# Kernel optimization log

Measured on AMD Instinct MI355X. Metric: run time of the kernel, lower is better.

The kernel has to match this reference:

```python
import jax, jax.numpy as jnp
import numpy as np

B, C, H, W = 8, 128, 128, 128
HEADS = 8

def setup_inputs() -> dict:
    key = jax.random.key(0)
    k1, k2 = jax.random.split(key)
    x1 = jax.random.normal(k1, (B, C, H, W), dtype=jnp.float32)
    x2 = jax.random.normal(k2, (B, C, H, W), dtype=jnp.float32)
    return {"x1": x1, "x2": x2}

def reference(x1, x2):
    b, c, h, w = x1.shape
    n = h * w
    hk = c // HEADS  # head key channels
    hv = c // HEADS  # head value channels
    # [B,C,N] layouts (channels-first, as in torch after transpose back)
    vals = x1.reshape(b, c, n)   # values come from x1
    kq = x2.reshape(b, c, n)     # keys and queries come from x2
    k = kq.reshape(b, HEADS, hk, n)
    v = vals.reshape(b, HEADS, hv, n)
    key_sm = jax.nn.softmax(k, axis=-1)   # softmax over N (torch dim=2)
    query_sm = jax.nn.softmax(k, axis=2)  # softmax over head channels (torch dim=1)
    # context = key @ value^T : [B,h,hk,hv]
    context = jnp.einsum('bhkn,bhvn->bhkv', key_sm, v)
    # attended = context^T @ query : [B,h,hv,N]
    attended = jnp.einsum('bhkv,bhkn->bhvn', context, query_sm)
    return attended.reshape(b, c, H, W)
```

## Files before the change

### kernel.cpp

```cpp
#include <hip/hip_runtime.h>
#include <math.h>

#define N_     16384
#define N4     4096
#define BHN    64
#define CH     16
#define CHUNKS 16

#define WS_PART 0
#define WS_ZP   (BHN * CHUNKS * 256)

typedef __attribute__((ext_vector_type(8))) short short8;
typedef __attribute__((ext_vector_type(4))) float f32x4;

static __device__ __forceinline__ short f2bf(float f) {
    __bf16 b = (__bf16)f;
    return __builtin_bit_cast(short, b);
}

__global__ __launch_bounds__(256) void k_ctx_mfma(const float* __restrict__ x1,
                                                  const float* __restrict__ x2,
                                                  float* __restrict__ ws) {
    int chunk = blockIdx.x;
    int bh    = blockIdx.y;
    int tid   = threadIdx.x;
    int w = tid >> 6, l = tid & 63;

    __shared__ __align__(16) short e_s[16][1032];
    __shared__ __align__(16) short v_s[16][1032];
    __shared__ float cred[4][256];
    __shared__ float zs[16];

    const float* xb2 = x2 + (size_t)bh * CH * N_ + chunk * 1024;
    const float* xb1 = x1 + (size_t)bh * CH * N_ + chunk * 1024;

    {
        int row = 4 * w;
        const float4* src = (const float4*)(xb2 + (size_t)row * N_);
        float4 a0 = src[l], a1 = src[64 + l], a2 = src[128 + l], a3 = src[192 + l];
        #pragma unroll
        for (int rr = 0; rr < 4; ++rr) {
            float4 b0 = a0, b1 = a1, b2 = a2, b3 = a3;
            if (rr < 3) {
                const float4* nx = (const float4*)(xb2 + (size_t)(row + rr + 1) * N_);
                a0 = nx[l]; a1 = nx[64 + l]; a2 = nx[128 + l]; a3 = nx[192 + l];
            }
            int r = row + rr;
            float e[16];
            e[0]=__expf(b0.x); e[1]=__expf(b0.y); e[2]=__expf(b0.z); e[3]=__expf(b0.w);
            e[4]=__expf(b1.x); e[5]=__expf(b1.y); e[6]=__expf(b1.z); e[7]=__expf(b1.w);
            e[8]=__expf(b2.x); e[9]=__expf(b2.y); e[10]=__expf(b2.z); e[11]=__expf(b2.w);
            e[12]=__expf(b3.x); e[13]=__expf(b3.y); e[14]=__expf(b3.z); e[15]=__expf(b3.w);
            float z = 0.f;
            #pragma unroll
            for (int i = 0; i < 16; ++i) z += e[i];
            #pragma unroll
            for (int off = 1; off < 64; off <<= 1) z += __shfl_xor(z, off);
            if (l == 0) zs[r] = z;
            #pragma unroll
            for (int s = 0; s < 4; ++s) {
                short4 pk = make_short4(f2bf(e[s*4]), f2bf(e[s*4+1]),
                                        f2bf(e[s*4+2]), f2bf(e[s*4+3]));
                *(short4*)&e_s[r][s * 256 + l * 4] = pk;
            }
        }
    }
    {
        int row = 4 * w;
        const float4* src = (const float4*)(xb1 + (size_t)row * N_);
        float4 a0 = src[l], a1 = src[64 + l], a2 = src[128 + l], a3 = src[192 + l];
        #pragma unroll
        for (int rr = 0; rr < 4; ++rr) {
            float4 b0 = a0, b1 = a1, b2 = a2, b3 = a3;
            if (rr < 3) {
                const float4* nx = (const float4*)(xb1 + (size_t)(row + rr + 1) * N_);
                a0 = nx[l]; a1 = nx[64 + l]; a2 = nx[128 + l]; a3 = nx[192 + l];
            }
            int r = row + rr;
            *(short4*)&v_s[r][0 * 256 + l * 4] = make_short4(f2bf(b0.x), f2bf(b0.y), f2bf(b0.z), f2bf(b0.w));
            *(short4*)&v_s[r][1 * 256 + l * 4] = make_short4(f2bf(b1.x), f2bf(b1.y), f2bf(b1.z), f2bf(b1.w));
            *(short4*)&v_s[r][2 * 256 + l * 4] = make_short4(f2bf(b2.x), f2bf(b2.y), f2bf(b2.z), f2bf(b2.w));
            *(short4*)&v_s[r][3 * 256 + l * 4] = make_short4(f2bf(b3.x), f2bf(b3.y), f2bf(b3.z), f2bf(b3.w));
        }
    }
    __syncthreads();

    int row16 = l & 15;
    int q     = l >> 4;
    f32x4 acc = {0.f, 0.f, 0.f, 0.f};
    #pragma unroll
    for (int s = 0; s < 8; ++s) {
        int col = w * 256 + s * 32 + q * 8;
        short8 af = *(const short8*)&e_s[row16][col];
        short8 bv = *(const short8*)&v_s[row16][col];
        acc = __builtin_amdgcn_mfma_f32_16x16x32_bf16(af, bv, acc, 0, 0, 0);
    }

    #pragma unroll
    for (int r = 0; r < 4; ++r)
        cred[w][(q * 4 + r) * 16 + row16] = acc[r];
    __syncthreads();

    if (tid < 16)
        ws[WS_ZP + (bh * CHUNKS + chunk) * 16 + tid] = zs[tid];
    float c = (cred[0][tid] + cred[1][tid]) + (cred[2][tid] + cred[3][tid]);
    ws[WS_PART + (size_t)(bh * CHUNKS + chunk) * 256 + tid] = c;
}

__global__ __launch_bounds__(256) void k_attend(const float* __restrict__ x2,
                                                const float* __restrict__ ws,
                                                float* __restrict__ out) {
    int cb  = blockIdx.x;
    int bh  = blockIdx.y;
    int tid = threadIdx.x;

    __shared__ float q_s[16][256];
    __shared__ float ctxs[256];
    __shared__ float rzs[16];

    float csum = 0.f;
    #pragma unroll
    for (int c = 0; c < CHUNKS; ++c)
        csum += ws[WS_PART + (size_t)(bh * CHUNKS + c) * 256 + tid];
    if (tid < 16) {
        float z = 0.f;
        #pragma unroll
        for (int c = 0; c < CHUNKS; ++c)
            z += ws[WS_ZP + (bh * CHUNKS + c) * 16 + tid];
        rzs[tid] = 1.0f / z;
    }

    const float4* px = (const float4*)(x2 + (size_t)bh * CH * N_);
    int base4 = cb * 64;
    #pragma unroll
    for (int r = 0; r < 4; ++r) {
        int idx = r * 256 + tid;
        int ch = idx >> 6, j = idx & 63;
        float4 v = px[(size_t)ch * N4 + base4 + j];
        *(float4*)&q_s[ch][j * 4] = v;
    }
    __syncthreads();

    ctxs[tid] = csum * rzs[tid >> 4];

    {
        int col = tid;
        float kv[16];
        #pragma unroll
        for (int c = 0; c < 16; ++c) kv[c] = q_s[c][col];
        float mx = kv[0];
        #pragma unroll
        for (int c = 1; c < 16; ++c) mx = fmaxf(mx, kv[c]);
        float s = 0.f;
        #pragma unroll
        for (int c = 0; c < 16; ++c) { kv[c] = __expf(kv[c] - mx); s += kv[c]; }
        float rs = 1.0f / s;
        #pragma unroll
        for (int c = 0; c < 16; ++c) q_s[c][col] = kv[c] * rs;
    }
    __syncthreads();

    int vg = tid >> 6, cq = tid & 63;
    int vv0 = vg * 4, c0 = cq * 4;
    float4 a0 = make_float4(0.f,0.f,0.f,0.f);
    float4 a1 = a0, a2 = a0, a3 = a0;
    #pragma unroll
    for (int kk = 0; kk < 16; ++kk) {
        float4 cx = *(const float4*)&ctxs[kk * 16 + vv0];
        float4 q4 = *(const float4*)&q_s[kk][c0];
        a0.x = fmaf(q4.x, cx.x, a0.x); a0.y = fmaf(q4.x, cx.y, a0.y);
        a0.z = fmaf(q4.x, cx.z, a0.z); a0.w = fmaf(q4.x, cx.w, a0.w);
        a1.x = fmaf(q4.y, cx.x, a1.x); a1.y = fmaf(q4.y, cx.y, a1.y);
        a1.z = fmaf(q4.y, cx.z, a1.z); a1.w = fmaf(q4.y, cx.w, a1.w);
        a2.x = fmaf(q4.z, cx.x, a2.x); a2.y = fmaf(q4.z, cx.y, a2.y);
        a2.z = fmaf(q4.z, cx.z, a2.z); a2.w = fmaf(q4.z, cx.w, a2.w);
        a3.x = fmaf(q4.w, cx.x, a3.x); a3.y = fmaf(q4.w, cx.y, a3.y);
        a3.z = fmaf(q4.w, cx.z, a3.z); a3.w = fmaf(q4.w, cx.w, a3.w);
    }
    size_t outbase = (size_t)bh * CH * N_ + (size_t)cb * 256 + c0;
    float4 o;
    o = make_float4(a0.x, a1.x, a2.x, a3.x);
    *(float4*)&out[outbase + (size_t)(vv0 + 0) * N_] = o;
    o = make_float4(a0.y, a1.y, a2.y, a3.y);
    *(float4*)&out[outbase + (size_t)(vv0 + 1) * N_] = o;
    o = make_float4(a0.z, a1.z, a2.z, a3.z);
    *(float4*)&out[outbase + (size_t)(vv0 + 2) * N_] = o;
    o = make_float4(a0.w, a1.w, a2.w, a3.w);
    *(float4*)&out[outbase + (size_t)(vv0 + 3) * N_] = o;
}

extern "C" void kernel_launch(void* const* d_in, const int* in_sizes, int n_in,
                              void* d_out, int out_size, void* d_ws, size_t ws_size,
                              hipStream_t stream) {
    const float* x1 = (const float*)d_in[0];
    const float* x2 = (const float*)d_in[1];
    float* out = (float*)d_out;
    float* ws  = (float*)d_ws;

    k_ctx_mfma <<<dim3(CHUNKS, BHN), 256, 0, stream>>>(x1, x2, ws);
    k_attend   <<<dim3(64, BHN),     256, 0, stream>>>(x2, ws, out);
}
```

Before: 52.03 us.

## Split context kernel into smaller chunks and specialize warps for key/value loading

Doubles the number of chunks per head so each block handles 512 columns instead of 1024, which halves shared memory and doubles the grid of the context kernel. Warps are specialized: two waves load and exponentiate x2 rows for keys while two waves convert x1 rows for values. All 16 loads per thread are issued up front into registers to raise memory-level parallelism. In exchange, the partial-sum workspace and the reduction loop in the attend kernel double in size.

Result: slower. 58.14 us (+11.8%).

```diff
diff --git a/kernel.cpp b/kernel.cpp
--- a/kernel.cpp
+++ b/kernel.cpp
@@ -5,7 +5,7 @@
 #define N4     4096
 #define BHN    64
 #define CH     16
-#define CHUNKS 16
+#define CHUNKS 32
 
 #define WS_PART 0
 #define WS_ZP   (BHN * CHUNKS * 256)
@@ -26,61 +26,46 @@
     int tid   = threadIdx.x;
     int w = tid >> 6, l = tid & 63;
 
-    __shared__ __align__(16) short e_s[16][1032];
-    __shared__ __align__(16) short v_s[16][1032];
+    __shared__ __align__(16) short e_s[16][520];
+    __shared__ __align__(16) short v_s[16][520];
     __shared__ float cred[4][256];
     __shared__ float zs[16];
 
-    const float* xb2 = x2 + (size_t)bh * CH * N_ + chunk * 1024;
-    const float* xb1 = x1 + (size_t)bh * CH * N_ + chunk * 1024;
+    {
+        const float* src = (w < 2) ? x2 : x1;
+        int r0 = (w & 1) * 8;
+        const float* base = src + (size_t)(bh * CH + r0) * N_ + chunk * 512;
 
-    {
-        int row = 4 * w;
-        const float4* src = (const float4*)(xb2 + (size_t)row * N_);
-        float4 a0 = src[l], a1 = src[64 + l], a2 = src[128 + l], a3 = src[192 + l];
+        float4 A[16];
         #pragma unroll
-        for (int rr = 0; rr < 4; ++rr) {
-            float4 b0 = a0, b1 = a1, b2 = a2, b3 = a3;
-            if (rr < 3) {
-                const float4* nx = (const float4*)(xb2 + (size_t)(row + rr + 1) * N_);
-                a0 = nx[l]; a1 = nx[64 + l]; a2 = nx[128 + l]; a3 = nx[192 + l];
+        for (int i = 0; i < 8; ++i) {
+            const float4* p = (const float4*)(base + (size_t)i * N_);
+            A[2 * i]     = p[2 * l];
+            A[2 * i + 1] = p[2 * l + 1];
+        }
+
+        if (w < 2) {
+            #pragma unroll
+            for (int i = 0; i < 8; ++i) {
+                float4 a = A[2 * i], b = A[2 * i + 1];
+                float e0 = __expf(a.x), e1 = __expf(a.y), e2 = __expf(a.z), e3 = __expf(a.w);
+                float e4 = __expf(b.x), e5 = __expf(b.y), e6 = __expf(b.z), e7 = __expf(b.w);
+                float z = ((e0 + e1) + (e2 + e3)) + ((e4 + e5) + (e6 + e7));
+                #pragma unroll
+                for (int off = 1; off < 64; off <<= 1) z += __shfl_xor(z, off);
+                if (l == 0) zs[r0 + i] = z;
+                short8 pk = {f2bf(e0), f2bf(e1), f2bf(e2), f2bf(e3),
+                             f2bf(e4), f2bf(e5), f2bf(e6), f2bf(e7)};
+                *(short8*)&e_s[r0 + i][l * 8] = pk;
             }
-            int r = row + rr;
-            float e[16];
-            e[0]=__expf(b0.x); e[1]=__expf(b0.y); e[2]=__expf(b0.z); e[3]=__expf(b0.w);
-            e[4]=__expf(b1.x); e[5]=__expf(b1.y); e[6]=__expf(b1.z); e[7]=__expf(b1.w);
-            e[8]=__expf(b2.x); e[9]=__expf(b2.y); e[10]=__expf(b2.z); e[11]=__expf(b2.w);
-            e[12]=__expf(b3.x); e[13]=__expf(b3.y); e[14]=__expf(b3.z); e[15]=__expf(b3.w);
-            float z = 0.f;
+        } else {
             #pragma unroll
-            for (int i = 0; i < 16; ++i) z += e[i];
-            #pragma unroll
-            for (int off = 1; off < 64; off <<= 1) z += __shfl_xor(z, off);
-            if (l == 0) zs[r] = z;
-            #pragma unroll
-            for (int s = 0; s < 4; ++s) {
-                short4 pk = make_short4(f2bf(e[s*4]), f2bf(e[s*4+1]),
-                                        f2bf(e[s*4+2]), f2bf(e[s*4+3]));
-                *(short4*)&e_s[r][s * 256 + l * 4] = pk;
+            for (int i = 0; i < 8; ++i) {
+                float4 a = A[2 * i], b = A[2 * i + 1];
+                short8 pv = {f2bf(a.x), f2bf(a.y), f2bf(a.z), f2bf(a.w),
+                             f2bf(b.x), f2bf(b.y), f2bf(b.z), f2bf(b.w)};
+                *(short8*)&v_s[r0 + i][l * 8] = pv;
             }
-        }
-    }
-    {
-        int row = 4 * w;
-        const float4* src = (const float4*)(xb1 + (size_t)row * N_);
-        float4 a0 = src[l], a1 = src[64 + l], a2 = src[128 + l], a3 = src[192 + l];
-        #pragma unroll
-        for (int rr = 0; rr < 4; ++rr) {
-            float4 b0 = a0, b1 = a1, b2 = a2, b3 = a3;
-            if (rr < 3) {
-                const float4* nx = (const float4*)(xb1 + (size_t)(row + rr + 1) * N_);
-                a0 = nx[l]; a1 = nx[64 + l]; a2 = nx[128 + l]; a3 = nx[192 + l];
-            }
-            int r = row + rr;
-            *(short4*)&v_s[r][0 * 256 + l * 4] = make_short4(f2bf(b0.x), f2bf(b0.y), f2bf(b0.z), f2bf(b0.w));
-            *(short4*)&v_s[r][1 * 256 + l * 4] = make_short4(f2bf(b1.x), f2bf(b1.y), f2bf(b1.z), f2bf(b1.w));
-            *(short4*)&v_s[r][2 * 256 + l * 4] = make_short4(f2bf(b2.x), f2bf(b2.y), f2bf(b2.z), f2bf(b2.w));
-            *(short4*)&v_s[r][3 * 256 + l * 4] = make_short4(f2bf(b3.x), f2bf(b3.y), f2bf(b3.z), f2bf(b3.w));
         }
     }
     __syncthreads();
@@ -89,8 +74,8 @@
     int q     = l >> 4;
     f32x4 acc = {0.f, 0.f, 0.f, 0.f};
     #pragma unroll
-    for (int s = 0; s < 8; ++s) {
-        int col = w * 256 + s * 32 + q * 8;
+    for (int s = 0; s < 4; ++s) {
+        int col = w * 128 + s * 32 + q * 8;
         short8 af = *(const short8*)&e_s[row16][col];
         short8 bv = *(const short8*)&v_s[row16][col];
         acc = __builtin_amdgcn_mfma_f32_16x16x32_bf16(af, bv, acc, 0, 0, 0);
```
